# Performance work log

Measured on AMD Instinct MI355X. Metric: run time of the kernel, lower is better.

Reference implementation:

```python
import jax, jax.numpy as jnp
import numpy as np

NH, DK, DV, D = 8, 64, 64, 768
DECAY = 0.95
WRITE_STRENGTH = 0.1


def setup_inputs() -> dict:
    key = jax.random.key(0)
    ks = jax.random.split(key, 6)
    s = 0.02  # small init scale for projection weights
    return {
        "x": jax.random.normal(ks[0], (4, 4096, D), dtype=jnp.float32),
        "w_key": jax.random.normal(ks[1], (NH * DK, D), dtype=jnp.float32) * s,
        "w_value": jax.random.normal(ks[2], (NH * DV, D), dtype=jnp.float32) * s,
        "w_query": jax.random.normal(ks[3], (NH * DK, D), dtype=jnp.float32) * s,
        "w_gate": jax.random.normal(ks[4], (NH, D), dtype=jnp.float32) * s,
        "w_out": jax.random.normal(ks[5], (D, NH * DV), dtype=jnp.float32) * s,
    }


def reference(x, w_key, w_value, w_query, w_gate, w_out):
    B, S, _ = x.shape
    # Batched projections (torch Linear: y = x @ W.T)
    k = (x @ w_key.T).reshape(B, S, NH, DK)
    v = (x @ w_value.T).reshape(B, S, NH, DV)
    q = (x @ w_query.T).reshape(B, S, NH, DK)
    gate = jax.nn.sigmoid(x @ w_gate.T)  # (B, S, NH)

    # Writes only use batch element 0 (mirrors k[0], v[0], gate[0] in source)
    k0 = k[0]      # (S, NH, DK)
    v0 = v[0]      # (S, NH, DV)
    g0 = gate[0]   # (S, NH)

    def step(fw, inp):
        q_t, k0_t, v0_t, g0_t = inp
        # Read BEFORE this step's decay+write
        retrieved = jnp.einsum('bhk,hkv->bhv', q_t, fw)  # (B, NH, DV)
        write = (WRITE_STRENGTH * g0_t)[:, None, None] * (k0_t[:, :, None] * v0_t[:, None, :])
        fw_new = DECAY * fw + jax.lax.stop_gradient(write)
        return fw_new, retrieved

    fw0 = jnp.zeros((NH, DK, DV), dtype=x.dtype)
    inputs = (q.transpose(1, 0, 2, 3), k0, v0, g0)  # time-major
    _, retrieved = jax.lax.scan(step, fw0, inputs)   # (S, B, NH, DV)
    retrieved = retrieved.transpose(1, 0, 2, 3).reshape(B, S, NH * DV)
    return x + retrieved @ w_out.T
```

## Files before the change

kernel.cpp:

```cpp
#include <hip/hip_runtime.h>
#include <hip/hip_bf16.h>

typedef __hip_bfloat16 bf16;
typedef __attribute__((ext_vector_type(8))) short   bf16x8;
typedef __attribute__((ext_vector_type(4))) float   f32x4;

#define B_   4
#define S_   4096
#define D_   768
#define NH_  8
#define DK_  64
#define DV_  64
#define CH_  64
#define NCH_ (S_/CH_)
#define DECAY_ 0.95f
#define WSTR_  0.1f

__device__ __forceinline__ float b2f(bf16 v) { return __bfloat162float(v); }
__device__ __forceinline__ bf16  f2b(float v) { return __float2bfloat16(v); }

__device__ __forceinline__ void gl2lds16(const bf16* g, bf16* lds) {
    __builtin_amdgcn_global_load_lds(
        (const __attribute__((address_space(1))) void*)g,
        (__attribute__((address_space(3))) void*)lds, 16, 0, 0);
}

__global__ __launch_bounds__(192) void cast_fused(const float* __restrict__ x,
                                                  bf16* __restrict__ xb,
                                                  const float* __restrict__ wg,
                                                  float* __restrict__ wgt,
                                                  const float* __restrict__ wq,
                                                  const float* __restrict__ wk,
                                                  const float* __restrict__ wv,
                                                  const float* __restrict__ wo,
                                                  bf16* __restrict__ dq, bf16* __restrict__ dk,
                                                  bf16* __restrict__ dv, bf16* __restrict__ dob) {
    const int tid = threadIdx.x;
    if (blockIdx.x >= (B_ * S_)) {
        const int idx = blockIdx.x - B_ * S_;
        const int which = idx >> 9, b = idx & 511;
        const float* src = which == 0 ? wq : which == 1 ? wk : which == 2 ? wv : wo;
        bf16*       dst = which == 0 ? dq : which == 1 ? dk : which == 2 ? dv : dob;
        const int i = (b * 192 + tid) * 4;
        const float4 v = *reinterpret_cast<const float4*>(src + i);
        union { bf16 b4[4]; ushort4 u; } t;
        t.b4[0] = f2b(v.x); t.b4[1] = f2b(v.y); t.b4[2] = f2b(v.z); t.b4[3] = f2b(v.w);
        *reinterpret_cast<ushort4*>(dst + i) = t.u;
        return;
    }
    const int s = blockIdx.x;
    const float4 v = *reinterpret_cast<const float4*>(x + (size_t)s * D_ + tid * 4);
    union { bf16 b4[4]; ushort4 u; } t;
    t.b4[0] = f2b(v.x); t.b4[1] = f2b(v.y); t.b4[2] = f2b(v.z); t.b4[3] = f2b(v.w);
    *reinterpret_cast<ushort4*>(xb + (size_t)s * D_ + tid * 4) = t.u;

    if (s < S_) {
        __shared__ float red[3 * 8];
        float p[8];
        const float* wgp = wg + tid * 4;
        #pragma unroll
        for (int h = 0; h < 8; h++) {
            const float4 wv4 = *reinterpret_cast<const float4*>(wgp + h * D_);
            p[h] = v.x * wv4.x + v.y * wv4.y + v.z * wv4.z + v.w * wv4.w;
        }
        #pragma unroll
        for (int h = 0; h < 8; h++)
            #pragma unroll
            for (int off = 32; off; off >>= 1) p[h] += __shfl_down(p[h], off);
        const int w = tid >> 6, lane = tid & 63;
        if (lane == 0) {
            #pragma unroll
            for (int h = 0; h < 8; h++) red[w * 8 + h] = p[h];
        }
        __syncthreads();
        if (tid < 8) {
            const float sum = red[tid] + red[8 + tid] + red[16 + tid];
            wgt[s * NH_ + tid] = WSTR_ / (1.f + expf(-sum));
        }
    }
}

template<typename TC, int ADDX, int NITER>
__device__ __forceinline__ void gemm_body(bf16* As, bf16* Bs,
                                          const bf16* __restrict__ A,
                                          const bf16* __restrict__ Bm,
                                          const float* __restrict__ X,
                                          TC* __restrict__ C,
                                          int bm, int bn, int K, int N) {
    const int tid = threadIdx.x, lane = tid & 63, w = tid >> 6;
    const int quad = lane >> 4, l16 = lane & 15;
    const int wm = (w >> 1) * 64, wn = (w & 1) * 64;
    const int lrow = lane >> 3;
    const int lcol = ((lane & 7) ^ lrow) * 8;

    f32x4 acc[4][4] = {};

    for (int it = 0; it < NITER; it++) {
        const int k0 = it * 64;
        #pragma unroll
        for (int c = 0; c < 4; c++) {
            const int seg = w * 4 + c;
            const int row = seg * 8 + lrow;
            gl2lds16(A  + (size_t)(bm + row) * K + k0 + lcol, &As[seg * 512]);
            gl2lds16(Bm + (size_t)(bn + row) * K + k0 + lcol, &Bs[seg * 512]);
        }
        __syncthreads();
        #pragma unroll
        for (int kh = 0; kh < 2; kh++) {
            bf16x8 af[4], bfr[4];
            #pragma unroll
            for (int t = 0; t < 4; t++) {
                const int cb = ((kh * 4 + quad) ^ (l16 & 7)) * 8;
                af[t]  = *reinterpret_cast<const bf16x8*>(&As[(wm + t * 16 + l16) * 64 + cb]);
                bfr[t] = *reinterpret_cast<const bf16x8*>(&Bs[(wn + t * 16 + l16) * 64 + cb]);
            }
            #pragma unroll
            for (int mt = 0; mt < 4; mt++)
                #pragma unroll
                for (int nt = 0; nt < 4; nt++)
                    acc[mt][nt] = __builtin_amdgcn_mfma_f32_16x16x32_bf16(
                        af[mt], bfr[nt], acc[mt][nt], 0, 0, 0);
        }
        __syncthreads();
    }

    #pragma unroll
    for (int mt = 0; mt < 4; mt++)
        #pragma unroll
        for (int nt = 0; nt < 4; nt++)
            #pragma unroll
            for (int r = 0; r < 4; r++) {
                const int m = bm + wm + mt * 16 + quad * 4 + r;
                const int n = bn + wn + nt * 16 + l16;
                float v = acc[mt][nt][r];
                if (ADDX) v += X[(size_t)m * N + n];
                if (sizeof(TC) == 2) *(bf16*)&C[(size_t)m * N + n] = f2b(v);
                else                 *(float*)&C[(size_t)m * N + n] = v;
            }
}

__global__ __launch_bounds__(256) void proj_fused(const bf16* __restrict__ xb,
                                                  const bf16* __restrict__ wqb,
                                                  const bf16* __restrict__ wkb,
                                                  const bf16* __restrict__ wvb,
                                                  bf16* __restrict__ qbuf,
                                                  bf16* __restrict__ k0buf,
                                                  bf16* __restrict__ v0buf) {
    __shared__ bf16 As[128 * 64];
    __shared__ bf16 Bs[128 * 64];
    const int id = blockIdx.x;
    const int xcd = id & 7;
    int j = id >> 3;
    const bf16* Bm; bf16* C; int bm, bn;
    if (j < 64) {
        bm = (xcd + ((j >> 2) << 3)) * 128;
        bn = (j & 3) * 128;
        Bm = wqb; C = qbuf;
    } else {
        j -= 64;
        bm = (xcd + ((j >> 3) << 3)) * 128;
        const int b8 = j & 7;
        bn = (b8 & 3) * 128;
        Bm = (b8 < 4) ? wkb : wvb;
        C  = (b8 < 4) ? k0buf : v0buf;
    }
    gemm_body<bf16, 0, 12>(As, Bs, xb, Bm, nullptr, C, bm, bn, D_, 512);
}

__global__ __launch_bounds__(256) void gemm_out(const bf16* __restrict__ retr,
                                                const bf16* __restrict__ wob,
                                                const float* __restrict__ x,
                                                float* __restrict__ out) {
    __shared__ bf16 As[128 * 64];
    __shared__ bf16 Bs[128 * 64];
    const int gx = gridDim.x, gy = gridDim.y;
    const int L = blockIdx.y * gx + blockIdx.x;
    const int rpx = gy >> 3;
    const int xcd = L & 7;
    const int i   = L >> 3;
    const int by = xcd * rpx + i / gx;
    const int bx = i % gx;
    gemm_body<float, 1, 8>(As, Bs, retr, wob, x, out, by * 128, bx * 128, 512, D_);
}

__global__ __launch_bounds__(256) void chunk_sums(const bf16* __restrict__ k0,
                                                  const bf16* __restrict__ v0,
                                                  const float* __restrict__ wgt,
                                                  bf16* __restrict__ lsumsT) {
    const int n = blockIdx.x, h = blockIdx.y;
    __shared__ float ks[CH_][65];
    __shared__ float vs[CH_][64];
    __shared__ float cw[CH_];
    const int tid = threadIdx.x;
    for (int e = tid; e < CH_ * 64; e += 256) {
        const int r = e >> 6, c = e & 63;
        const int t = n * CH_ + r;
        ks[r][c] = b2f(k0[(size_t)t * (NH_ * DK_) + h * DK_ + c]);
        vs[r][c] = b2f(v0[(size_t)t * (NH_ * DV_) + h * DV_ + c]);
    }
    if (tid < CH_) {
        const int t = n * CH_ + tid;
        cw[tid] = powf(DECAY_, (float)(CH_ - 1 - tid)) * wgt[t * NH_ + h];
    }
    __syncthreads();
    const int j = tid & 63, ig = tid >> 6;
    float acc[16] = {};
    for (int idx = 0; idx < CH_; idx++) {
        const float ck = cw[idx] * ks[idx][j];
        #pragma unroll
        for (int r = 0; r < 16; r++) acc[r] += vs[idx][ig * 16 + r] * ck;
    }
    bf16* outp = lsumsT + ((size_t)(n * NH_ + h)) * (DK_ * DV_);
    #pragma unroll
    for (int r = 0; r < 16; r++) outp[(ig * 16 + r) * 64 + j] = f2b(acc[r]);
}

__device__ __forceinline__ void cvt4(ushort4 u, float f[4]) {
    union { unsigned u; float f; } c;
    c.u = (unsigned)u.x << 16; f[0] = c.f;
    c.u = (unsigned)u.y << 16; f[1] = c.f;
    c.u = (unsigned)u.z << 16; f[2] = c.f;
    c.u = (unsigned)u.w << 16; f[3] = c.f;
}

__global__ __launch_bounds__(256) void chunk_output(const bf16* __restrict__ q,
                                                    const bf16* __restrict__ k0,
                                                    const bf16* __restrict__ v0,
                                                    const float* __restrict__ wgt,
                                                    const bf16* __restrict__ lsumsT,
                                                    bf16* __restrict__ retr) {
    const int n = blockIdx.x, h = blockIdx.y, b = blockIdx.z;
    __shared__ bf16 QsVT[64 * 72];
    __shared__ bf16 KsAm[64 * 72];
    __shared__ bf16 FWT[64 * 64];
    __shared__ float dpow[64], winv[64];
    const int tid = threadIdx.x, lane = tid & 63, w = tid >> 6;
    const int quad = lane >> 4, l16 = lane & 15;
    const int t0 = n * CH_;
    const int lrow = lane >> 3;
    const int lcol = ((lane & 7) ^ lrow) * 8;

    #pragma unroll
    for (int c = 0; c < 2; c++) {
        const int seg = w * 2 + c;
        const int row = seg * 8 + lrow;
        gl2lds16(q  + ((size_t)(b * S_ + t0 + row)) * 512 + h * 64 + lcol, &QsVT[seg * 512]);
        gl2lds16(k0 + ((size_t)(t0 + row)) * 512 + h * 64 + lcol,          &KsAm[seg * 512]);
    }
    {
        float fwacc[16] = {};
        const float dcp[4] = { 1.0f, 0.0375241f, 1.40806e-3f, 5.28365e-5f };
        #pragma unroll
        for (int jj = 1; jj <= 4; jj++) {
            const int nm = n - jj;
            if (nm < 0) break;
            const ushort* Lp = (const ushort*)(lsumsT + ((size_t)(nm * NH_ + h)) * 4096) + tid * 16;
            #pragma unroll
            for (int u = 0; u < 4; u++) {
                float f[4];
                cvt4(reinterpret_cast<const ushort4*>(Lp)[u], f);
                #pragma unroll
                for (int e = 0; e < 4; e++) fwacc[u * 4 + e] += dcp[jj - 1] * f[e];
            }
        }
        const int frow = tid >> 2;
        #pragma unroll
        for (int half = 0; half < 2; half++) {
            const int cb = (tid & 3) * 2 + half;
            union { bf16 b8v[8]; bf16x8 v; } t;
            #pragma unroll
            for (int e = 0; e < 8; e++) t.b8v[e] = f2b(fwacc[half * 8 + e]);
            *reinterpret_cast<bf16x8*>(&FWT[frow * 64 + (cb ^ (frow & 7)) * 8]) = t.v;
        }
    }
    ushort4 vreg[4];
    const int jb = (tid & 15) * 4;
    const int sb = tid >> 4;
    #pragma unroll
    for (int it = 0; it < 4; it++) {
        vreg[it] = *reinterpret_cast<const ushort4*>(
            v0 + ((size_t)(t0 + sb + it * 16)) * 512 + h * 64 + jb);
    }
    if (tid < 64) {
        dpow[tid] = powf(DECAY_, (float)tid);
        winv[tid] = wgt[(t0 + tid) * NH_ + h] * powf(DECAY_, -(float)(tid + 1));
    }
    __syncthreads();

    const int mrow = w * 16;
    float dpow_tt[4], winv_l[4];
    #pragma unroll
    for (int r = 0; r < 4; r++) dpow_tt[r] = dpow[mrow + quad * 4 + r];
    #pragma unroll
    for (int nt = 0; nt < 4; nt++) winv_l[nt] = winv[nt * 16 + l16];

    const int cb0 = ((quad) ^ (l16 & 7)) * 8;
    const int cb1 = ((4 + quad) ^ (l16 & 7)) * 8;
    const bf16x8 af0 = *reinterpret_cast<const bf16x8*>(&QsVT[(mrow + l16) * 64 + cb0]);
    const bf16x8 af1 = *reinterpret_cast<const bf16x8*>(&QsVT[(mrow + l16) * 64 + cb1]);
    f32x4 acc[4] = {};
    #pragma unroll
    for (int nt = 0; nt < 4; nt++) {
        const bf16x8 b0 = *reinterpret_cast<const bf16x8*>(&KsAm[(nt * 16 + l16) * 64 + cb0]);
        const bf16x8 b1 = *reinterpret_cast<const bf16x8*>(&KsAm[(nt * 16 + l16) * 64 + cb1]);
        acc[nt] = __builtin_amdgcn_mfma_f32_16x16x32_bf16(af0, b0, acc[nt], 0, 0, 0);
        acc[nt] = __builtin_amdgcn_mfma_f32_16x16x32_bf16(af1, b1, acc[nt], 0, 0, 0);
    }
    __syncthreads();

    #pragma unroll
    for (int nt = 0; nt < 4; nt++) {
        const int s = nt * 16 + l16;
        #pragma unroll
        for (int r = 0; r < 4; r++) {
            const int tt = mrow + quad * 4 + r;
            const float v = (s < tt) ? acc[nt][r] * dpow_tt[r] * winv_l[nt] : 0.f;
            KsAm[tt * 72 + s] = f2b(v);
        }
    }
    {
        ushort* VT = reinterpret_cast<ushort*>(QsVT);
        #pragma unroll
        for (int it = 0; it < 4; it++) {
            const int s = sb + it * 16;
            VT[(jb + 0) * 72 + s] = vreg[it].x;
            VT[(jb + 1) * 72 + s] = vreg[it].y;
            VT[(jb + 2) * 72 + s] = vreg[it].z;
            VT[(jb + 3) * 72 + s] = vreg[it].w;
        }
    }
    __syncthreads();

    f32x4 o[4] = {};
    #pragma unroll
    for (int nt = 0; nt < 4; nt++) {
        const bf16x8 f0 = *reinterpret_cast<const bf16x8*>(&FWT[(nt * 16 + l16) * 64 + cb0]);
        const bf16x8 f1 = *reinterpret_cast<const bf16x8*>(&FWT[(nt * 16 + l16) * 64 + cb1]);
        o[nt] = __builtin_amdgcn_mfma_f32_16x16x32_bf16(af0, f0, o[nt], 0, 0, 0);
        o[nt] = __builtin_amdgcn_mfma_f32_16x16x32_bf16(af1, f1, o[nt], 0, 0, 0);
    }
    #pragma unroll
    for (int nt = 0; nt < 4; nt++)
        #pragma unroll
        for (int r = 0; r < 4; r++) o[nt][r] *= dpow_tt[r];

    const bf16x8 a0 = *reinterpret_cast<const bf16x8*>(&KsAm[(mrow + l16) * 72 + quad * 8]);
    const bf16x8 a1 = *reinterpret_cast<const bf16x8*>(&KsAm[(mrow + l16) * 72 + 32 + quad * 8]);
    #pragma unroll
    for (int nt = 0; nt < 4; nt++) {
        const bf16x8 v0f = *reinterpret_cast<const bf16x8*>(&QsVT[(nt * 16 + l16) * 72 + quad * 8]);
        const bf16x8 v1f = *reinterpret_cast<const bf16x8*>(&QsVT[(nt * 16 + l16) * 72 + 32 + quad * 8]);
        o[nt] = __builtin_amdgcn_mfma_f32_16x16x32_bf16(a0, v0f, o[nt], 0, 0, 0);
        o[nt] = __builtin_amdgcn_mfma_f32_16x16x32_bf16(a1, v1f, o[nt], 0, 0, 0);
    }
    #pragma unroll
    for (int nt = 0; nt < 4; nt++)
        #pragma unroll
        for (int r = 0; r < 4; r++) {
            const int tt = mrow + quad * 4 + r;
            retr[((size_t)(b * S_ + t0 + tt)) * 512 + h * 64 + nt * 16 + l16] = f2b(o[nt][r]);
        }
}

extern "C" void kernel_launch(void* const* d_in, const int* in_sizes, int n_in,
                              void* d_out, int out_size, void* d_ws, size_t ws_size,
                              hipStream_t stream) {
    const float* x  = (const float*)d_in[0];
    const float* wk = (const float*)d_in[1];
    const float* wv = (const float*)d_in[2];
    const float* wq = (const float*)d_in[3];
    const float* wg = (const float*)d_in[4];
    const float* wo = (const float*)d_in[5];
    float* out = (float*)d_out;

    const size_t MB1 = 1ull << 20;
    char* w = (char*)d_ws;
    bf16*  qbuf    = (bf16*)(w);
    bf16*  k0buf   = (bf16*)(w + 16 * MB1);
    bf16*  v0buf   = (bf16*)(w + 20 * MB1);
    float* wgt     = (float*)(w + 24 * MB1);
    bf16*  wqb     = (bf16*)(w + 24 * MB1 + (128ull<<10));
    bf16*  wkb     = (bf16*)(w + 24 * MB1 + (128ull<<10) + 1*786432);
    bf16*  wvb     = (bf16*)(w + 24 * MB1 + (128ull<<10) + 2*786432);
    bf16*  wob     = (bf16*)(w + 24 * MB1 + (128ull<<10) + 3*786432);
    bf16*  lsumsT  = (bf16*)(w + 28 * MB1);
    bf16*  retr    = (bf16*)(w + 32 * MB1);
    bf16*  xb      = (bf16*)(w + 48 * MB1);

    const int MB = B_ * S_;

    cast_fused<<<MB + 2048, 192, 0, stream>>>(x, xb, wg, wgt,
                                              wq, wk, wv, wo, wqb, wkb, wvb, wob);

    proj_fused<<<768, 256, 0, stream>>>(xb, wqb, wkb, wvb, qbuf, k0buf, v0buf);

    chunk_sums<<<dim3(NCH_, NH_), 256, 0, stream>>>(k0buf, v0buf, wgt, lsumsT);
    chunk_output<<<dim3(NCH_, NH_, B_), 256, 0, stream>>>(qbuf, k0buf, v0buf, wgt, lsumsT, retr);

    gemm_out<<<dim3(D_ / 128, MB / 128), 256, 0, stream>>>(retr, wob, x, out);
}
```

Before: 204.7 us.

## Process all batches per block in chunk_output to share K, V and state

Each chunk_output block now handles all four batch elements, one per wave, instead of launching a separate block per batch. K, V, the carried fast-weight state and the decay weights are loaded and prepared once and reused across batches. Each wave computes a full 64x64 tile with more MFMAs and registers. The grid shrinks by four, which reduces parallelism, and LDS use and register pressure grow.

```diff
diff --git a/kernel.cpp b/kernel.cpp
--- a/kernel.cpp
+++ b/kernel.cpp
@@ -229,10 +229,11 @@
                                                     const float* __restrict__ wgt,
                                                     const bf16* __restrict__ lsumsT,
                                                     bf16* __restrict__ retr) {
-    const int n = blockIdx.x, h = blockIdx.y, b = blockIdx.z;
-    __shared__ bf16 QsVT[64 * 72];
-    __shared__ bf16 KsAm[64 * 72];
+    const int n = blockIdx.x, h = blockIdx.y;
+    __shared__ bf16 QsAm[4][64 * 64];
+    __shared__ bf16 Ks[64 * 64];
     __shared__ bf16 FWT[64 * 64];
+    __shared__ bf16 VT[64 * 72];
     __shared__ float dpow[64], winv[64];
     const int tid = threadIdx.x, lane = tid & 63, w = tid >> 6;
     const int quad = lane >> 4, l16 = lane & 15;
@@ -241,12 +242,17 @@
     const int lcol = ((lane & 7) ^ lrow) * 8;
 
     #pragma unroll
+    for (int seg = 0; seg < 8; seg++) {
+        const int row = seg * 8 + lrow;
+        gl2lds16(q + ((size_t)(w * S_ + t0 + row)) * 512 + h * 64 + lcol, &QsAm[w][seg * 512]);
+    }
+    #pragma unroll
     for (int c = 0; c < 2; c++) {
         const int seg = w * 2 + c;
         const int row = seg * 8 + lrow;
-        gl2lds16(q  + ((size_t)(b * S_ + t0 + row)) * 512 + h * 64 + lcol, &QsVT[seg * 512]);
-        gl2lds16(k0 + ((size_t)(t0 + row)) * 512 + h * 64 + lcol,          &KsAm[seg * 512]);
-    }
+        gl2lds16(k0 + ((size_t)(t0 + row)) * 512 + h * 64 + lcol, &Ks[seg * 512]);
+    }
+
     {
         float fwacc[16] = {};
         const float dcp[4] = { 1.0f, 0.0375241f, 1.40806e-3f, 5.28365e-5f };
@@ -273,13 +279,23 @@
             *reinterpret_cast<bf16x8*>(&FWT[frow * 64 + (cb ^ (frow & 7)) * 8]) = t.v;
         }
     }
-    ushort4 vreg[4];
-    const int jb = (tid & 15) * 4;
-    const int sb = tid >> 4;
-    #pragma unroll
-    for (int it = 0; it < 4; it++) {
-        vreg[it] = *reinterpret_cast<const ushort4*>(
-            v0 + ((size_t)(t0 + sb + it * 16)) * 512 + h * 64 + jb);
+    {
+        ushort4 vreg[4];
+        const int jb = (tid & 15) * 4;
+        const int sb = tid >> 4;
+        #pragma unroll
+        for (int it = 0; it < 4; it++)
+            vreg[it] = *reinterpret_cast<const ushort4*>(
+                v0 + ((size_t)(t0 + sb + it * 16)) * 512 + h * 64 + jb);
+        ushort* VTu = reinterpret_cast<ushort*>(VT);
+        #pragma unroll
+        for (int it = 0; it < 4; it++) {
+            const int s = sb + it * 16;
+            VTu[(jb + 0) * 72 + s] = vreg[it].x;
+            VTu[(jb + 1) * 72 + s] = vreg[it].y;
+            VTu[(jb + 2) * 72 + s] = vreg[it].z;
+            VTu[(jb + 3) * 72 + s] = vreg[it].w;
+        }
     }
     if (tid < 64) {
         dpow[tid] = powf(DECAY_, (float)tid);
@@ -287,79 +303,101 @@
     }
     __syncthreads();
 
-    const int mrow = w * 16;
-    float dpow_tt[4], winv_l[4];
-    #pragma unroll
-    for (int r = 0; r < 4; r++) dpow_tt[r] = dpow[mrow + quad * 4 + r];
-    #pragma unroll
-    for (int nt = 0; nt < 4; nt++) winv_l[nt] = winv[nt * 16 + l16];
-
     const int cb0 = ((quad) ^ (l16 & 7)) * 8;
     const int cb1 = ((4 + quad) ^ (l16 & 7)) * 8;
-    const bf16x8 af0 = *reinterpret_cast<const bf16x8*>(&QsVT[(mrow + l16) * 64 + cb0]);
-    const bf16x8 af1 = *reinterpret_cast<const bf16x8*>(&QsVT[(mrow + l16) * 64 + cb1]);
-    f32x4 acc[4] = {};
-    #pragma unroll
-    for (int nt = 0; nt < 4; nt++) {
-        const bf16x8 b0 = *reinterpret_cast<const bf16x8*>(&KsAm[(nt * 16 + l16) * 64 + cb0]);
-        const bf16x8 b1 = *reinterpret_cast<const bf16x8*>(&KsAm[(nt * 16 + l16) * 64 + cb1]);
-        acc[nt] = __builtin_amdgcn_mfma_f32_16x16x32_bf16(af0, b0, acc[nt], 0, 0, 0);
-        acc[nt] = __builtin_amdgcn_mfma_f32_16x16x32_bf16(af1, b1, acc[nt], 0, 0, 0);
-    }
-    __syncthreads();
-
-    #pragma unroll
-    for (int nt = 0; nt < 4; nt++) {
-        const int s = nt * 16 + l16;
-        #pragma unroll
-        for (int r = 0; r < 4; r++) {
-            const int tt = mrow + quad * 4 + r;
-            const float v = (s < tt) ? acc[nt][r] * dpow_tt[r] * winv_l[nt] : 0.f;
-            KsAm[tt * 72 + s] = f2b(v);
-        }
-    }
-    {
-        ushort* VT = reinterpret_cast<ushort*>(QsVT);
-        #pragma unroll
-        for (int it = 0; it < 4; it++) {
-            const int s = sb + it * 16;
-            VT[(jb + 0) * 72 + s] = vreg[it].x;
-            VT[(jb + 1) * 72 + s] = vreg[it].y;
-            VT[(jb + 2) * 72 + s] = vreg[it].z;
-            VT[(jb + 3) * 72 + s] = vreg[it].w;
-        }
-    }
-    __syncthreads();
-
-    f32x4 o[4] = {};
-    #pragma unroll
-    for (int nt = 0; nt < 4; nt++) {
-        const bf16x8 f0 = *reinterpret_cast<const bf16x8*>(&FWT[(nt * 16 + l16) * 64 + cb0]);
-        const bf16x8 f1 = *reinterpret_cast<const bf16x8*>(&FWT[(nt * 16 + l16) * 64 + cb1]);
-        o[nt] = __builtin_amdgcn_mfma_f32_16x16x32_bf16(af0, f0, o[nt], 0, 0, 0);
-        o[nt] = __builtin_amdgcn_mfma_f32_16x16x32_bf16(af1, f1, o[nt], 0, 0, 0);
-    }
-    #pragma unroll
-    for (int nt = 0; nt < 4; nt++)
-        #pragma unroll
-        for (int r = 0; r < 4; r++) o[nt][r] *= dpow_tt[r];
-
-    const bf16x8 a0 = *reinterpret_cast<const bf16x8*>(&KsAm[(mrow + l16) * 72 + quad * 8]);
-    const bf16x8 a1 = *reinterpret_cast<const bf16x8*>(&KsAm[(mrow + l16) * 72 + 32 + quad * 8]);
-    #pragma unroll
-    for (int nt = 0; nt < 4; nt++) {
-        const bf16x8 v0f = *reinterpret_cast<const bf16x8*>(&QsVT[(nt * 16 + l16) * 72 + quad * 8]);
-        const bf16x8 v1f = *reinterpret_cast<const bf16x8*>(&QsVT[(nt * 16 + l16) * 72 + 32 + quad * 8]);
-        o[nt] = __builtin_amdgcn_mfma_f32_16x16x32_bf16(a0, v0f, o[nt], 0, 0, 0);
-        o[nt] = __builtin_amdgcn_mfma_f32_16x16x32_bf16(a1, v1f, o[nt], 0, 0, 0);
-    }
-    #pragma unroll
-    for (int nt = 0; nt < 4; nt++)
-        #pragma unroll
-        for (int r = 0; r < 4; r++) {
-            const int tt = mrow + quad * 4 + r;
-            retr[((size_t)(b * S_ + t0 + tt)) * 512 + h * 64 + nt * 16 + l16] = f2b(o[nt][r]);
-        }
+    bf16* Qw = &QsAm[w][0];
+
+    bf16x8 af[4][2];
+    #pragma unroll
+    for (int mt = 0; mt < 4; mt++) {
+        af[mt][0] = *reinterpret_cast<const bf16x8*>(&Qw[(mt * 16 + l16) * 64 + cb0]);
+        af[mt][1] = *reinterpret_cast<const bf16x8*>(&Qw[(mt * 16 + l16) * 64 + cb1]);
+    }
+
+    f32x4 acc[4][4] = {};
+    #pragma unroll
+    for (int kh = 0; kh < 2; kh++) {
+        bf16x8 bk[4];
+        #pragma unroll
+        for (int nt = 0; nt < 4; nt++)
+            bk[nt] = *reinterpret_cast<const bf16x8*>(
+                &Ks[(nt * 16 + l16) * 64 + (kh ? cb1 : cb0)]);
+        #pragma unroll
+        for (int mt = 0; mt < 4; mt++)
+            #pragma unroll
+            for (int nt = 0; nt < 4; nt++)
+                acc[mt][nt] = __builtin_amdgcn_mfma_f32_16x16x32_bf16(
+                    af[mt][kh], bk[nt], acc[mt][nt], 0, 0, 0);
+    }
+
+    const float pmt[4] = { 1.0f, 0.4401266694f, 0.1937114891f, 0.0852578070f };
+    const f32x4 dpb = *reinterpret_cast<const f32x4*>(&dpow[quad * 4]);
+    float winv_l[4];
+    #pragma unroll
+    for (int nt = 0; nt < 4; nt++) winv_l[nt] = winv[nt * 16 + l16];
+    #pragma unroll
+    for (int mt = 0; mt < 4; mt++)
+        #pragma unroll
+        for (int nt = 0; nt < 4; nt++)
+            #pragma unroll
+            for (int r = 0; r < 4; r++) {
+                const int tt = mt * 16 + quad * 4 + r;
+                const int s = nt * 16 + l16;
+                const float v = (s < tt) ? acc[mt][nt][r] * (dpb[r] * pmt[mt]) * winv_l[nt] : 0.f;
+                Qw[tt * 64 + (((s >> 3) ^ (tt & 7)) << 3) + (s & 7)] = f2b(v);
+            }
+
+    f32x4 o[4][4] = {};
+    #pragma unroll
+    for (int kh = 0; kh < 2; kh++) {
+        bf16x8 ff[4];
+        #pragma unroll
+        for (int nt = 0; nt < 4; nt++)
+            ff[nt] = *reinterpret_cast<const bf16x8*>(
+                &FWT[(nt * 16 + l16) * 64 + (kh ? cb1 : cb0)]);
+        #pragma unroll
+        for (int mt = 0; mt < 4; mt++)
+            #pragma unroll
+            for (int nt = 0; nt < 4; nt++)
+                o[mt][nt] = __builtin_amdgcn_mfma_f32_16x16x32_bf16(
+                    af[mt][kh], ff[nt], o[mt][nt], 0, 0, 0);
+    }
+    #pragma unroll
+    for (int mt = 0; mt < 4; mt++)
+        #pragma unroll
+        for (int nt = 0; nt < 4; nt++)
+            #pragma unroll
+            for (int r = 0; r < 4; r++) o[mt][nt][r] *= dpb[r] * pmt[mt];
+
+    #pragma unroll
+    for (int kh = 0; kh < 2; kh++) {
+        bf16x8 am[4], vf[4];
+        #pragma unroll
+        for (int mt = 0; mt < 4; mt++)
+            am[mt] = *reinterpret_cast<const bf16x8*>(
+                &Qw[(mt * 16 + l16) * 64 + (kh ? cb1 : cb0)]);
+        #pragma unroll
+        for (int nt = 0; nt < 4; nt++)
+            vf[nt] = *reinterpret_cast<const bf16x8*>(
+                &VT[(nt * 16 + l16) * 72 + kh * 32 + quad * 8]);
+        #pragma unroll
+        for (int mt = 0; mt < 4; mt++)
+            #pragma unroll
+            for (int nt = 0; nt < 4; nt++)
+                o[mt][nt] = __builtin_amdgcn_mfma_f32_16x16x32_bf16(
+                    am[mt], vf[nt], o[mt][nt], 0, 0, 0);
+    }
+
+    #pragma unroll
+    for (int mt = 0; mt < 4; mt++)
+        #pragma unroll
+        for (int nt = 0; nt < 4; nt++)
+            #pragma unroll
+            for (int r = 0; r < 4; r++) {
+                const int tt = mt * 16 + quad * 4 + r;
+                retr[((size_t)(w * S_ + t0 + tt)) * 512 + h * 64 + nt * 16 + l16] =
+                    f2b(o[mt][nt][r]);
+            }
 }
 
 extern "C" void kernel_launch(void* const* d_in, const int* in_sizes, int n_in,
@@ -395,7 +433,7 @@
     proj_fused<<<768, 256, 0, stream>>>(xb, wqb, wkb, wvb, qbuf, k0buf, v0buf);
 
     chunk_sums<<<dim3(NCH_, NH_), 256, 0, stream>>>(k0buf, v0buf, wgt, lsumsT);
-    chunk_output<<<dim3(NCH_, NH_, B_), 256, 0, stream>>>(qbuf, k0buf, v0buf, wgt, lsumsT, retr);
+    chunk_output<<<dim3(NCH_, NH_), 256, 0, stream>>>(qbuf, k0buf, v0buf, wgt, lsumsT, retr);
 
     gemm_out<<<dim3(D_ / 128, MB / 128), 256, 0, stream>>>(retr, wob, x, out);
 }
```

After: 196.2 us. 4.1% less time.
